# Kernel optimization log

Measured on AMD Instinct MI355X. Metric: run time of the kernel, lower is better.

The kernel has to match this reference:

```python
import jax, jax.numpy as jnp
import numpy as np

B, M, H = 16, 2048, 1024
THRESHOLD = 0.99  # hardcoded in the torch module regardless of the init arg


def _unpack(x, run):
    """Scatter left-packed rows of x back to full width M, zeros at exited slots.
    x: [B, M, H] (row b's first run[b].sum() columns are live tokens)
    run: [B, M] bool."""
    src = jnp.cumsum(run, axis=1) - 1              # packed-source index per live slot
    src = jnp.where(run, src, 0)
    gathered = jnp.take_along_axis(x, src[:, :, None], axis=1)  # [B,M,H]
    return gathered * run[:, :, None]


def _pack(x, run):
    """Left-compact live tokens of x per row; trailing slots zero.
    Equivalent to the torch pack() padded out to full width M (torch pads only
    to the per-batch max live count; the extra columns here are zeros)."""
    dest = jnp.cumsum(run, axis=1) - 1
    dest = jnp.where(run, dest, M)                 # exited tokens go to overflow slot
    out = jnp.zeros((B, M + 1, H), x.dtype)
    out = out.at[jnp.arange(B)[:, None], dest].set(x * run[:, :, None])
    return out[:, :M]


def setup_inputs() -> dict:
    key = jax.random.key(0)
    k = jax.random.split(key, 6)
    h = jax.random.normal(k[0], (B, M, H), dtype=jnp.float32)
    weighted_h = jax.random.normal(k[1], (B, M, H), dtype=jnp.float32) * 0.1
    acc_p = jax.random.uniform(k[2], (B, M, 1), dtype=jnp.float32, maxval=0.9)
    remainders = jnp.zeros((B, M, 1), jnp.float32)
    p_weight = jax.random.normal(k[3], (1, H), dtype=jnp.float32) / np.sqrt(H)
    p_bias = jnp.zeros((1,), jnp.float32)
    run = jax.random.bernoulli(k[4], 0.7, (B, M))
    exit_ = jnp.zeros((B, M, 1), jnp.int32)
    updates = 3
    return dict(h=h, weighted_h=weighted_h, acc_p=acc_p, remainders=remainders,
                p_weight=p_weight, p_bias=p_bias, run=run, exit_=exit_, updates=updates)


def reference(h, weighted_h, acc_p, remainders, p_weight, p_bias, run, exit_, updates):
    run3 = run[:, :, None]                          # [B,M,1] bool
    run_f = run3.astype(h.dtype)
    hu = _unpack(h, run)                            # [B,M,H]
    # halting prob; zero at already-exited positions
    p = jax.nn.sigmoid(jnp.einsum('bmh,oh->bmo', hu, p_weight) + p_bias) * run_f
    acc_new = acc_p + p                             # torch updates acc_p in place first
    mask_continue = (acc_new < THRESHOLD) & run3
    mask_exit = (~mask_continue) & run3
    mc_f = mask_continue.astype(h.dtype)
    me_f = mask_exit.astype(h.dtype)
    # exit branch uses remainder 1 - old_acc_p  (acc_new - p == old acc_p)
    p_eff = p * mc_f + (1.0 - (acc_new - p)) * me_f
    weighted_h_new = hu * p_eff + weighted_h * (1.0 - p_eff)
    run_new = run & mask_continue[:, :, 0]
    remainders_new = remainders + p_eff * me_f
    updates_new = updates + 1
    exit_new = exit_ + updates_new * mask_exit.astype(exit_.dtype)
    h_packed = _pack(hu, run_new)
    return h_packed, weighted_h_new, acc_new, remainders_new, run_new, exit_new
```

## Files before the change

### kernel.cpp

```cpp
#include <hip/hip_runtime.h>
#include <math.h>

#define Bq 16
#define Mq 2048
#define Hq 1024
#define BMQ (Bq * Mq)
static constexpr float THR = 0.99f;

typedef float f4v __attribute__((ext_vector_type(4)));

__device__ __forceinline__ void nt_store4(float* p, float x, float y, float z,
                                          float w) {
  f4v t = {x, y, z, w};
  __builtin_nontemporal_store(t, (f4v*)p);
}
__device__ __forceinline__ f4v nt_load4(const float* p) {
  return __builtin_nontemporal_load((const f4v*)p);
}

#define GRID_G 2048
__global__ __launch_bounds__(256) void k_gemv(const float* __restrict__ h,
                                              const float* __restrict__ pw,
                                              const float* __restrict__ pb,
                                              const int* __restrict__ run,
                                              float* __restrict__ logits) {
  int wv = threadIdx.x >> 6, lane = threadIdx.x & 63;
  int b0 = blockIdx.x >> 9;
  __shared__ int s_nl[4];
  {
    const int* rr = run + (b0 + 4 * wv) * Mq;
    int c = 0;
#pragma unroll
    for (int i = 0; i < Mq / 64; ++i) c += rr[(i << 6) + lane];
#pragma unroll
    for (int off = 32; off; off >>= 1) c += __shfl_xor(c, off);
    if (lane == 0) s_nl[wv] = c;
  }
  const float4* w4 = (const float4*)pw;
  float4 w[4];
#pragma unroll
  for (int k = 0; k < 4; ++k) w[k] = w4[(k << 6) + lane];
  float bias = pb[0];
  __syncthreads();
#pragma unroll
  for (int i = 0; i < 4; ++i) {
    int task = (blockIdx.x << 2) + wv + (i << 13);
    int r = task & (Mq - 1);
    if (r < s_nl[i]) {
      const float4* hrow = (const float4*)(h + ((size_t)task) * Hq);
      float s = 0.f;
#pragma unroll
      for (int k = 0; k < 4; ++k) {
        float4 a = hrow[(k << 6) + lane];
        s += a.x * w[k].x + a.y * w[k].y + a.z * w[k].z + a.w * w[k].w;
      }
#pragma unroll
      for (int off = 32; off; off >>= 1) s += __shfl_xor(s, off);
      if (lane == 0) logits[task] = s + bias;
    }
  }
}

#define SCAN_T 1024
__device__ __forceinline__ int wave_scan(int v, int lane) {
#pragma unroll
  for (int off = 1; off < 64; off <<= 1) {
    int n = __shfl_up(v, off);
    if (lane >= off) v += n;
  }
  return v;
}

__global__ __launch_bounds__(SCAN_T) void k_scan(
    const float* __restrict__ accp, const float* __restrict__ rem,
    const int* __restrict__ run, const int* __restrict__ exin,
    const int* __restrict__ upd, const float* __restrict__ logits,
    float* __restrict__ out_acc, float* __restrict__ out_rem,
    float* __restrict__ out_run, float* __restrict__ out_exit,
    int* __restrict__ rank_ws, float* __restrict__ peff_ws,
    int* __restrict__ pdest_ws) {
  int b = blockIdx.x;
  int tid = threadIdx.x;
  int lane = tid & 63, wv = tid >> 6;
  __shared__ int wsA[16], wsB[16];
  int carry_run = 0, carry_cont = 0;
  int unew = upd[0] + 1;
  for (int chunk = 0; chunk < Mq; chunk += SCAN_T) {
    int m = chunk + tid;
    int idx = b * Mq + m;
    int r = run[idx];
    int incl = wave_scan(r, lane);
    if (lane == 63) wsA[wv] = incl;
    __syncthreads();
    int pre = 0, tot = 0;
#pragma unroll
    for (int i = 0; i < 16; ++i) { int t = wsA[i]; if (i < wv) pre += t; tot += t; }
    incl += pre;
    int rank = carry_run + incl - 1;
    float p = 0.f;
    if (r) {
      float z = logits[b * Mq + rank];
      if (z >= 0.f) p = 1.f / (1.f + expf(-z));
      else { float e = expf(z); p = e / (1.f + e); }
    }
    float accn = accp[idx] + p;
    int cont = (int)(accn < THR) & r;
    int ex = r & (cont ^ 1);
    float diff = accn - p;
    float peff = cont ? p : (ex ? (1.0f - diff) : 0.0f);
    out_acc[idx] = accn;
    out_rem[idx] = rem[idx] + (ex ? peff : 0.0f);
    out_run[idx] = cont ? 1.0f : 0.0f;
    out_exit[idx] = (float)(exin[idx] + (ex ? unew : 0));
    rank_ws[idx] = r ? rank : -1;
    peff_ws[idx] = peff;
    int inclc = wave_scan(cont, lane);
    if (lane == 63) wsB[wv] = inclc;
    __syncthreads();
    int prec = 0, totc = 0;
#pragma unroll
    for (int i = 0; i < 16; ++i) { int t = wsB[i]; if (i < wv) prec += t; totc += t; }
    inclc += prec;
    if (cont) {
      pdest_ws[idx] = carry_cont + inclc - 1;
    } else {
      int zr = m - (carry_cont + inclc);
      pdest_ws[idx] = -(Mq - 1 - zr) - 1;
    }
    carry_run += tot;
    carry_cont += totc;
  }
}

#define GRID_A 2048
__global__ __launch_bounds__(256) void k_apply(
    const float* __restrict__ h, const float* __restrict__ wh,
    const int* __restrict__ rank_ws, const float* __restrict__ peff_ws,
    const int* __restrict__ pdest_ws,
    float* __restrict__ out_hp, float* __restrict__ out_wh) {
  int tid = threadIdx.x;
  for (int bm = blockIdx.x; bm < BMQ; bm += GRID_A) {
    int b = bm >> 11;
    size_t rowoff = (size_t)bm * Hq;
    int rk = rank_ws[bm];
    int pd = pdest_ws[bm];
    float pe = peff_ws[bm];
    f4v w4 = nt_load4(wh + rowoff + 4 * tid);
    float ax = 0.f, ay = 0.f, az = 0.f, aw = 0.f;
    float ox, oy, oz, ow;
    if (rk >= 0) {
      const float4* hrow = (const float4*)(h + ((size_t)(b * Mq + rk)) * Hq);
      float4 a = hrow[tid];
      ax = a.x; ay = a.y; az = a.z; aw = a.w;
      float q = 1.0f - pe;
      ox = ax * pe + w4.x * q;
      oy = ay * pe + w4.y * q;
      oz = az * pe + w4.z * q;
      ow = aw * pe + w4.w * q;
    } else {
      ox = w4.x; oy = w4.y; oz = w4.z; ow = w4.w;
    }
    nt_store4(out_wh + rowoff + 4 * tid, ox, oy, oz, ow);
    if (pd >= 0) {
      nt_store4(out_hp + (((size_t)(b * Mq + pd)) * Hq) + 4 * tid, ax, ay, az, aw);
    } else {
      int zd = -(pd + 1);
      nt_store4(out_hp + (((size_t)(b * Mq + zd)) * Hq) + 4 * tid, 0.f, 0.f, 0.f,
                0.f);
    }
  }
}

extern "C" void kernel_launch(void* const* d_in, const int* in_sizes, int n_in,
                              void* d_out, int out_size, void* d_ws, size_t ws_size,
                              hipStream_t stream) {
  const float* h    = (const float*)d_in[0];
  const float* wh   = (const float*)d_in[1];
  const float* accp = (const float*)d_in[2];
  const float* rem  = (const float*)d_in[3];
  const float* pw   = (const float*)d_in[4];
  const float* pb   = (const float*)d_in[5];
  const int*   run  = (const int*)d_in[6];
  const int*   exin = (const int*)d_in[7];
  const int*   upd  = (const int*)d_in[8];

  float* out = (float*)d_out;
  const size_t BMH = (size_t)Bq * Mq * Hq;
  const size_t BM  = (size_t)Bq * Mq;
  float* out_hp   = out;
  float* out_wh   = out + BMH;
  float* out_acc  = out + 2 * BMH;
  float* out_rem  = out_acc + BM;
  float* out_run  = out_rem + BM;
  float* out_exit = out_run + BM;

  float* logits  = (float*)d_ws;
  int*   rank_ws = (int*)d_ws + BM;
  float* peff_ws = (float*)d_ws + 2 * BM;
  int*   pdest_ws= (int*)d_ws + 3 * BM;

  k_gemv<<<GRID_G, 256, 0, stream>>>(h, pw, pb, run, logits);
  k_scan<<<Bq, SCAN_T, 0, stream>>>(accp, rem, run, exin, upd, logits,
                                    out_acc, out_rem, out_run, out_exit,
                                    rank_ws, peff_ws, pdest_ws);
  k_apply<<<GRID_A, 256, 0, stream>>>(h, wh, rank_ws, peff_ws, pdest_ws,
                                      out_hp, out_wh);
}
```

Baseline: 444.6 us.

## Fuse gemv, scan and apply into one cooperative kernel with grid syncs

Replaces the three launches (gemv, per-batch scan, apply) with a single cooperative kernel of 1024 blocks that separates the phases with grid-wide syncs. The scan phase now runs on only 16 blocks of 256 threads instead of 1024-thread blocks, so each batch row takes 8 serial chunks. The goal is to remove launch gaps and inter-kernel drain between phases. In exchange, the rest of the grid idles during the scan, the scan itself is narrower, and the apply loop runs on fewer blocks than before.

```diff
diff --git a/kernel.cpp b/kernel.cpp
--- a/kernel.cpp
+++ b/kernel.cpp
@@ -1,10 +1,14 @@
 #include <hip/hip_runtime.h>
+#include <hip/hip_cooperative_groups.h>
 #include <math.h>
+
+namespace cg = cooperative_groups;
 
 #define Bq 16
 #define Mq 2048
 #define Hq 1024
 #define BMQ (Bq * Mq)
+#define NBLK 1024
 static constexpr float THR = 0.99f;
 
 typedef float f4v __attribute__((ext_vector_type(4)));
@@ -18,50 +22,6 @@
   return __builtin_nontemporal_load((const f4v*)p);
 }
 
-#define GRID_G 2048
-__global__ __launch_bounds__(256) void k_gemv(const float* __restrict__ h,
-                                              const float* __restrict__ pw,
-                                              const float* __restrict__ pb,
-                                              const int* __restrict__ run,
-                                              float* __restrict__ logits) {
-  int wv = threadIdx.x >> 6, lane = threadIdx.x & 63;
-  int b0 = blockIdx.x >> 9;
-  __shared__ int s_nl[4];
-  {
-    const int* rr = run + (b0 + 4 * wv) * Mq;
-    int c = 0;
-#pragma unroll
-    for (int i = 0; i < Mq / 64; ++i) c += rr[(i << 6) + lane];
-#pragma unroll
-    for (int off = 32; off; off >>= 1) c += __shfl_xor(c, off);
-    if (lane == 0) s_nl[wv] = c;
-  }
-  const float4* w4 = (const float4*)pw;
-  float4 w[4];
-#pragma unroll
-  for (int k = 0; k < 4; ++k) w[k] = w4[(k << 6) + lane];
-  float bias = pb[0];
-  __syncthreads();
-#pragma unroll
-  for (int i = 0; i < 4; ++i) {
-    int task = (blockIdx.x << 2) + wv + (i << 13);
-    int r = task & (Mq - 1);
-    if (r < s_nl[i]) {
-      const float4* hrow = (const float4*)(h + ((size_t)task) * Hq);
-      float s = 0.f;
-#pragma unroll
-      for (int k = 0; k < 4; ++k) {
-        float4 a = hrow[(k << 6) + lane];
-        s += a.x * w[k].x + a.y * w[k].y + a.z * w[k].z + a.w * w[k].w;
-      }
-#pragma unroll
-      for (int off = 32; off; off >>= 1) s += __shfl_xor(s, off);
-      if (lane == 0) logits[task] = s + bias;
-    }
-  }
-}
-
-#define SCAN_T 1024
 __device__ __forceinline__ int wave_scan(int v, int lane) {
 #pragma unroll
   for (int off = 1; off < 64; off <<= 1) {
@@ -71,75 +31,113 @@
   return v;
 }
 
-__global__ __launch_bounds__(SCAN_T) void k_scan(
+__global__ __launch_bounds__(256, 4) void k_fused(
+    const float* __restrict__ h, const float* __restrict__ wh,
     const float* __restrict__ accp, const float* __restrict__ rem,
+    const float* __restrict__ pw, const float* __restrict__ pb,
     const int* __restrict__ run, const int* __restrict__ exin,
-    const int* __restrict__ upd, const float* __restrict__ logits,
+    const int* __restrict__ upd,
+    float* __restrict__ out_hp, float* __restrict__ out_wh,
     float* __restrict__ out_acc, float* __restrict__ out_rem,
     float* __restrict__ out_run, float* __restrict__ out_exit,
-    int* __restrict__ rank_ws, float* __restrict__ peff_ws,
-    int* __restrict__ pdest_ws) {
-  int b = blockIdx.x;
+    float* __restrict__ logits, int* __restrict__ rank_ws,
+    float* __restrict__ peff_ws, int* __restrict__ pdest_ws) {
+  cg::grid_group grid = cg::this_grid();
   int tid = threadIdx.x;
   int lane = tid & 63, wv = tid >> 6;
-  __shared__ int wsA[16], wsB[16];
-  int carry_run = 0, carry_cont = 0;
-  int unew = upd[0] + 1;
-  for (int chunk = 0; chunk < Mq; chunk += SCAN_T) {
-    int m = chunk + tid;
-    int idx = b * Mq + m;
-    int r = run[idx];
-    int incl = wave_scan(r, lane);
-    if (lane == 63) wsA[wv] = incl;
+  int blk = blockIdx.x;
+
+  {
+    int b = blk >> 6;
+    int r0 = (blk & 63) << 5;
+    const int* rr = run + b * Mq;
+    int c = 0;
+#pragma unroll
+    for (int i = 0; i < 8; ++i) c += rr[(i << 8) + tid];
+#pragma unroll
+    for (int off = 32; off; off >>= 1) c += __shfl_xor(c, off);
+    __shared__ int s_c[4];
+    if (lane == 0) s_c[wv] = c;
     __syncthreads();
-    int pre = 0, tot = 0;
-#pragma unroll
-    for (int i = 0; i < 16; ++i) { int t = wsA[i]; if (i < wv) pre += t; tot += t; }
-    incl += pre;
-    int rank = carry_run + incl - 1;
-    float p = 0.f;
-    if (r) {
-      float z = logits[b * Mq + rank];
-      if (z >= 0.f) p = 1.f / (1.f + expf(-z));
-      else { float e = expf(z); p = e / (1.f + e); }
-    }
-    float accn = accp[idx] + p;
-    int cont = (int)(accn < THR) & r;
-    int ex = r & (cont ^ 1);
-    float diff = accn - p;
-    float peff = cont ? p : (ex ? (1.0f - diff) : 0.0f);
-    out_acc[idx] = accn;
-    out_rem[idx] = rem[idx] + (ex ? peff : 0.0f);
-    out_run[idx] = cont ? 1.0f : 0.0f;
-    out_exit[idx] = (float)(exin[idx] + (ex ? unew : 0));
-    rank_ws[idx] = r ? rank : -1;
-    peff_ws[idx] = peff;
-    int inclc = wave_scan(cont, lane);
-    if (lane == 63) wsB[wv] = inclc;
-    __syncthreads();
-    int prec = 0, totc = 0;
-#pragma unroll
-    for (int i = 0; i < 16; ++i) { int t = wsB[i]; if (i < wv) prec += t; totc += t; }
-    inclc += prec;
-    if (cont) {
-      pdest_ws[idx] = carry_cont + inclc - 1;
-    } else {
-      int zr = m - (carry_cont + inclc);
-      pdest_ws[idx] = -(Mq - 1 - zr) - 1;
-    }
-    carry_run += tot;
-    carry_cont += totc;
-  }
-}
-
-#define GRID_A 2048
-__global__ __launch_bounds__(256) void k_apply(
-    const float* __restrict__ h, const float* __restrict__ wh,
-    const int* __restrict__ rank_ws, const float* __restrict__ peff_ws,
-    const int* __restrict__ pdest_ws,
-    float* __restrict__ out_hp, float* __restrict__ out_wh) {
-  int tid = threadIdx.x;
-  for (int bm = blockIdx.x; bm < BMQ; bm += GRID_A) {
+    int nl = s_c[0] + s_c[1] + s_c[2] + s_c[3];
+    const float4* w4p = (const float4*)pw;
+    float4 w[4];
+#pragma unroll
+    for (int k = 0; k < 4; ++k) w[k] = w4p[(k << 6) + lane];
+    float bias = pb[0];
+#pragma unroll
+    for (int it = 0; it < 8; ++it) {
+      int r = r0 + (it << 2) + wv;
+      if (r < nl) {
+        const float4* hrow = (const float4*)(h + ((size_t)(b * Mq + r)) * Hq);
+        float s = 0.f;
+#pragma unroll
+        for (int k = 0; k < 4; ++k) {
+          float4 a = hrow[(k << 6) + lane];
+          s += a.x * w[k].x + a.y * w[k].y + a.z * w[k].z + a.w * w[k].w;
+        }
+#pragma unroll
+        for (int off = 32; off; off >>= 1) s += __shfl_xor(s, off);
+        if (lane == 0) logits[b * Mq + r] = s + bias;
+      }
+    }
+  }
+  grid.sync();
+
+  if (blk < Bq) {
+    int b = blk;
+    __shared__ int wsA[4], wsB[4];
+    int carry_run = 0, carry_cont = 0;
+    int unew = upd[0] + 1;
+    for (int chunk = 0; chunk < Mq; chunk += 256) {
+      int m = chunk + tid;
+      int idx = b * Mq + m;
+      int r = run[idx];
+      int incl = wave_scan(r, lane);
+      if (lane == 63) wsA[wv] = incl;
+      __syncthreads();
+      int pre = 0, tot = 0;
+#pragma unroll
+      for (int i = 0; i < 4; ++i) { int t = wsA[i]; if (i < wv) pre += t; tot += t; }
+      incl += pre;
+      int rank = carry_run + incl - 1;
+      float p = 0.f;
+      if (r) {
+        float z = logits[b * Mq + rank];
+        if (z >= 0.f) p = 1.f / (1.f + expf(-z));
+        else { float e = expf(z); p = e / (1.f + e); }
+      }
+      float accn = accp[idx] + p;
+      int cont = (int)(accn < THR) & r;
+      int ex = r & (cont ^ 1);
+      float diff = accn - p;
+      float peff = cont ? p : (ex ? (1.0f - diff) : 0.0f);
+      out_acc[idx] = accn;
+      out_rem[idx] = rem[idx] + (ex ? peff : 0.0f);
+      out_run[idx] = cont ? 1.0f : 0.0f;
+      out_exit[idx] = (float)(exin[idx] + (ex ? unew : 0));
+      rank_ws[idx] = r ? rank : -1;
+      peff_ws[idx] = peff;
+      int inclc = wave_scan(cont, lane);
+      if (lane == 63) wsB[wv] = inclc;
+      __syncthreads();
+      int prec = 0, totc = 0;
+#pragma unroll
+      for (int i = 0; i < 4; ++i) { int t = wsB[i]; if (i < wv) prec += t; totc += t; }
+      inclc += prec;
+      if (cont) {
+        pdest_ws[idx] = carry_cont + inclc - 1;
+      } else {
+        int zr = m - (carry_cont + inclc);
+        pdest_ws[idx] = -(Mq - 1 - zr) - 1;
+      }
+      carry_run += tot;
+      carry_cont += totc;
+    }
+  }
+  grid.sync();
+
+  for (int bm = blk; bm < BMQ; bm += NBLK) {
     int b = bm >> 11;
     size_t rowoff = (size_t)bm * Hq;
     int rk = rank_ws[bm];
@@ -199,10 +197,12 @@
   float* peff_ws = (float*)d_ws + 2 * BM;
   int*   pdest_ws= (int*)d_ws + 3 * BM;
 
-  k_gemv<<<GRID_G, 256, 0, stream>>>(h, pw, pb, run, logits);
-  k_scan<<<Bq, SCAN_T, 0, stream>>>(accp, rem, run, exin, upd, logits,
-                                    out_acc, out_rem, out_run, out_exit,
-                                    rank_ws, peff_ws, pdest_ws);
-  k_apply<<<GRID_A, 256, 0, stream>>>(h, wh, rank_ws, peff_ws, pdest_ws,
-                                      out_hp, out_wh);
-}
+  void* kargs[] = {
+      (void*)&h,       (void*)&wh,      (void*)&accp,   (void*)&rem,
+      (void*)&pw,      (void*)&pb,      (void*)&run,    (void*)&exin,
+      (void*)&upd,     (void*)&out_hp,  (void*)&out_wh, (void*)&out_acc,
+      (void*)&out_rem, (void*)&out_run, (void*)&out_exit,
+      (void*)&logits,  (void*)&rank_ws, (void*)&peff_ws, (void*)&pdest_ws};
+  hipLaunchCooperativeKernel((void*)k_fused, dim3(NBLK), dim3(256), kargs, 0,
+                             stream);
+}
```

Measured after the change: 692.5 us. +55.7%, slower.
